# Kernel optimization log

Measured on AMD Instinct MI355X. Metric: run time of the kernel, lower is better.

Reference implementation:

```python
import jax, jax.numpy as jnp
import numpy as np


def _rope(x, fr, fi):
    # Faithful port of apply_rotary_embeddings: deinterleave even/odd elements,
    # reshape to (-1, *fr.shape), rotate, then concat halves and reshape back.
    shp = x.shape
    dims = fr.shape  # (seq_len, 1, head_dim//2)
    xf = x.reshape(-1, 2)
    xr = xf[:, 0].reshape((-1,) + dims)
    xi = xf[:, 1].reshape((-1,) + dims)
    out_r = xr * fr - xi * fi
    out_i = xr * fi + xi * fr
    return jnp.concatenate([out_r, out_i], axis=-1).reshape(shp).astype(x.dtype)


def setup_inputs() -> dict:
    key = jax.random.key(0)
    ks = jax.random.split(key, 9)
    B, S, Dm, H, Hd, P = 16, 1, 4096, 32, 128, 2048
    W = 0.02  # weight scale to keep score magnitudes sane
    return {
        "x": jax.random.normal(ks[0], (B, S, Dm), jnp.float32),
        "cache_k": jax.random.normal(ks[1], (B, P, H, Hd), jnp.float32),
        "cache_v": jax.random.normal(ks[2], (B, P, H, Hd), jnp.float32),
        "freqs_real": jax.random.normal(ks[3], (S, 1, Hd // 2), jnp.float32),
        "freqs_imag": jax.random.normal(ks[4], (S, 1, Hd // 2), jnp.float32),
        "dwq": jax.random.normal(ks[5], (Dm, Dm), jnp.float32) * W,
        "dwk": jax.random.normal(ks[6], (Dm, Dm), jnp.float32) * W,
        "dwv": jax.random.normal(ks[7], (Dm, Dm), jnp.float32) * W,
        "dwo": jax.random.normal(ks[8], (Dm, Dm), jnp.float32) * W,
        "start_pos": P,
    }


def reference(x, cache_k, cache_v, freqs_real, freqs_imag, dwq, dwk, dwv, dwo, start_pos):
    B, S, _ = x.shape
    H, Hd = cache_k.shape[2], cache_k.shape[3]
    scale = 1.0 / np.float32(np.sqrt(Hd))

    xq = (x @ dwq.T).reshape(B, S, H, Hd)
    xk = (x @ dwk.T).reshape(B, S, H, Hd)
    xv = (x @ dwv.T).reshape(B, S, H, Hd)
    xq = _rope(xq, freqs_real, freqs_imag)
    xk = _rope(xk, freqs_real, freqs_imag)

    # KV-cache append (cat-based growth in the original)
    keys = jnp.concatenate([cache_k, xk], axis=1)      # (B, P+S, H, Hd)
    values = jnp.concatenate([cache_v, xv], axis=1)

    q = xq.transpose(0, 2, 1, 3)       # (B, H, S, Hd)
    k = keys.transpose(0, 2, 1, 3)     # (B, H, P+S, Hd)
    v = values.transpose(0, 2, 1, 3)

    scores = jnp.einsum('bhqd,bhkd->bhqk', q, k) * scale
    probs = jax.nn.softmax(scores.astype(jnp.float32), axis=-1).astype(q.dtype)
    out = jnp.einsum('bhqk,bhkd->bhqd', probs, v)
    out = out.transpose(0, 2, 1, 3).reshape(B, S, H * Hd)
    return out @ dwo.T  # allreduce is identity with tp=1
```

## Files before the change

### kernel.cpp

```cpp
#include <hip/hip_runtime.h>
#include <cstdint>

#define DM 4096
#define NB 16
#define NH 32
#define HD 128
#define PP 2048
#define NCHUNK 32
#define CROWS 64
#define PSTRIDE 132
#define KP 256
#define NPAN (DM / KP)

typedef __attribute__((ext_vector_type(8))) short bf16x8;
typedef __attribute__((ext_vector_type(4))) float f32x4;

__device__ inline f32x4 ntld4(const float* p) {
  return __builtin_nontemporal_load(reinterpret_cast<const f32x4*>(p));
}

__device__ inline void split_pair(float x0, float x1, uint32_t& hpair,
                                  uint32_t& lpair) {
  uint32_t u0 = __float_as_uint(x0), u1 = __float_as_uint(x1);
  hpair = __builtin_amdgcn_perm(u1, u0, 0x07060302u);
  float l0 = x0 - __uint_as_float(u0 & 0xFFFF0000u);
  float l1 = x1 - __uint_as_float(u1 & 0xFFFF0000u);
  asm("v_cvt_pk_bf16_f32 %0, %1, %2" : "=v"(lpair) : "v"(l0), "v"(l1));
}

template <bool ROPE>
__device__ inline void gemv16(const float* __restrict__ A,
                              const float* __restrict__ W,
                              float* __restrict__ O, int jt,
                              const float* __restrict__ fr,
                              const float* __restrict__ fi) {
  const int wave = threadIdx.x >> 6;
  const int lane = threadIdx.x & 63;
  const int m = lane & 15;
  const int kg = lane >> 4;
  const float* arow = A + (size_t)m * DM;

  __shared__ float wt[2][16][KP + 4];
  __shared__ float red[4][256];

  f32x4 acc = {0.f, 0.f, 0.f, 0.f};

  {
    f32x4 s0[4];
#pragma unroll
    for (int j = 0; j < 4; ++j) {
      const int row = wave * 4 + j;
      s0[j] = ntld4(W + (size_t)(jt + row) * DM + lane * 4);
    }
#pragma unroll
    for (int j = 0; j < 4; ++j) {
      const int row = wave * 4 + j;
      *(f32x4*)&wt[0][row][lane * 4] = s0[j];
    }
  }
  __syncthreads();

  int buf = 0;
  for (int p = 0; p < NPAN; ++p) {
    f32x4 stg[4];
    if (p + 1 < NPAN) {
#pragma unroll
      for (int j = 0; j < 4; ++j) {
        const int row = wave * 4 + j;
        stg[j] = ntld4(W + (size_t)(jt + row) * DM + (p + 1) * KP + lane * 4);
      }
    }
#pragma unroll
    for (int s = 0; s < 2; ++s) {
      const int kl = (wave << 6) + (s << 5) + kg * 8;
      f32x4 wa = *(const f32x4*)&wt[buf][m][kl];
      f32x4 wb = *(const f32x4*)&wt[buf][m][kl + 4];
      f32x4 xa = *(const f32x4*)(arow + p * KP + kl);
      f32x4 xb = *(const f32x4*)(arow + p * KP + kl + 4);
      union { bf16x8 v; uint32_t d[4]; } ah, al, wh, wl;
      split_pair(xa.x, xa.y, ah.d[0], al.d[0]);
      split_pair(xa.z, xa.w, ah.d[1], al.d[1]);
      split_pair(xb.x, xb.y, ah.d[2], al.d[2]);
      split_pair(xb.z, xb.w, ah.d[3], al.d[3]);
      split_pair(wa.x, wa.y, wh.d[0], wl.d[0]);
      split_pair(wa.z, wa.w, wh.d[1], wl.d[1]);
      split_pair(wb.x, wb.y, wh.d[2], wl.d[2]);
      split_pair(wb.z, wb.w, wh.d[3], wl.d[3]);
      acc = __builtin_amdgcn_mfma_f32_16x16x32_bf16(ah.v, wh.v, acc, 0, 0, 0);
      acc = __builtin_amdgcn_mfma_f32_16x16x32_bf16(ah.v, wl.v, acc, 0, 0, 0);
      acc = __builtin_amdgcn_mfma_f32_16x16x32_bf16(al.v, wh.v, acc, 0, 0, 0);
    }
    if (p + 1 < NPAN) {
#pragma unroll
      for (int j = 0; j < 4; ++j) {
        const int row = wave * 4 + j;
        *(f32x4*)&wt[buf ^ 1][row][lane * 4] = stg[j];
      }
    }
    __syncthreads();
    buf ^= 1;
  }

  red[wave][lane * 4 + 0] = acc[0];
  red[wave][lane * 4 + 1] = acc[1];
  red[wave][lane * 4 + 2] = acc[2];
  red[wave][lane * 4 + 3] = acc[3];
  __syncthreads();
  const int t = threadIdx.x;
  float s = red[0][t] + red[1][t] + red[2][t] + red[3][t];
  float part = 0.f;
  if (ROPE) {
    __syncthreads();
    red[0][t] = s;
    __syncthreads();
    part = red[0][t ^ 4];
  }
  const int l = t >> 2, r = t & 3;
  const int bb = ((l >> 4) << 2) + r;
  const int n = l & 15;
  const int c = jt + n;
  float val;
  int oc;
  if (ROPE) {
    const int j = (c & 127) >> 1;
    const float f_r = fr[j], f_i = fi[j];
    if ((c & 1) == 0) {
      val = s * f_r - part * f_i;
      oc = (c & ~127) + j;
    } else {
      val = part * f_i + s * f_r;
      oc = (c & ~127) + 64 + j;
    }
  } else {
    val = s;
    oc = c;
  }
  O[(size_t)bb * DM + oc] = val;
}

__global__ __launch_bounds__(256) void qkv_proj_kernel(
    const float* __restrict__ x, const float* __restrict__ wq,
    const float* __restrict__ wk, const float* __restrict__ wv,
    const float* __restrict__ fr, const float* __restrict__ fi,
    float* __restrict__ oq, float* __restrict__ ok, float* __restrict__ ov) {
  const int g = blockIdx.x >> 8;
  const int jt = (blockIdx.x & 255) << 4;
  if (g == 0)
    gemv16<true>(x, wq, oq, jt, fr, fi);
  else if (g == 1)
    gemv16<true>(x, wk, ok, jt, fr, fi);
  else
    gemv16<false>(x, wv, ov, jt, nullptr, nullptr);
}

__global__ __launch_bounds__(256) void oproj_kernel(
    const float* __restrict__ a, const float* __restrict__ w,
    float* __restrict__ o) {
  gemv16<false>(a, w, o, blockIdx.x << 4, nullptr, nullptr);
}

__global__ __launch_bounds__(512) void attn_chunk_kernel(
    const float* __restrict__ qrope, const float* __restrict__ cache_k,
    const float* __restrict__ cache_v, float* __restrict__ part) {
  const int b = blockIdx.x >> 5;
  const int c = blockIdx.x & 31;
  const int t = threadIdx.x;
  __shared__ float sc[NH][CROWS];

  const f32x4 qa = *(const f32x4*)(qrope + (size_t)b * DM + 4 * t);
  const f32x4 qb = *(const f32x4*)(qrope + (size_t)b * DM + 2048 + 4 * t);
  const int h1 = t >> 5;
  const int h2 = h1 + 16;
  const float scale = 0.08838834764831845f;

  const float* Kb = cache_k + ((size_t)b * PP + (size_t)c * CROWS) * DM;
#pragma unroll 2
  for (int r = 0; r < CROWS; ++r) {
    const float* krow = Kb + (size_t)r * DM + 4 * t;
    f32x4 k1 = ntld4(krow);
    f32x4 k2 = ntld4(krow + 2048);
    float p1 = qa.x * k1.x + qa.y * k1.y + qa.z * k1.z + qa.w * k1.w;
    float p2 = qb.x * k2.x + qb.y * k2.y + qb.z * k2.z + qb.w * k2.w;
#pragma unroll
    for (int off = 1; off <= 16; off <<= 1) {
      p1 += __shfl_xor(p1, off);
      p2 += __shfl_xor(p2, off);
    }
    if ((t & 31) == 0) {
      sc[h1][r] = p1 * scale;
      sc[h2][r] = p2 * scale;
    }
  }
  __syncthreads();

  const int hh = t >> 4, u = t & 15;
  float4 sv4 = *(const float4*)(&sc[hh][u * 4]);
  float mx = fmaxf(fmaxf(sv4.x, sv4.y), fmaxf(sv4.z, sv4.w));
#pragma unroll
  for (int off = 1; off <= 8; off <<= 1) mx = fmaxf(mx, __shfl_xor(mx, off));
  float e0 = __expf(sv4.x - mx), e1 = __expf(sv4.y - mx);
  float e2 = __expf(sv4.z - mx), e3 = __expf(sv4.w - mx);
  float4 ev = {e0, e1, e2, e3};
  *(float4*)(&sc[hh][u * 4]) = ev;
  float sm = (e0 + e1) + (e2 + e3);
#pragma unroll
  for (int off = 1; off <= 8; off <<= 1) sm += __shfl_xor(sm, off);
  float* pb = part + ((size_t)(b * NCHUNK + c) * NH) * PSTRIDE;
  if (u == 0) {
    pb[hh * PSTRIDE + 128] = mx;
    pb[hh * PSTRIDE + 129] = sm;
  }
  __syncthreads();

  const float* Vb = cache_v + ((size_t)b * PP + (size_t)c * CROWS) * DM;
  f32x4 a1 = {0.f, 0.f, 0.f, 0.f}, a2 = {0.f, 0.f, 0.f, 0.f};
#pragma unroll 2
  for (int r = 0; r < CROWS; ++r) {
    const float* vrow = Vb + (size_t)r * DM + 4 * t;
    f32x4 v1 = ntld4(vrow);
    f32x4 v2 = ntld4(vrow + 2048);
    float w1 = sc[h1][r], w2 = sc[h2][r];
    a1 += w1 * v1;
    a2 += w2 * v2;
  }
  const int dbase = (4 * t) & 127;
  *(f32x4*)(pb + h1 * PSTRIDE + dbase) = a1;
  *(f32x4*)(pb + h2 * PSTRIDE + dbase) = a2;
}

__global__ __launch_bounds__(128) void attn_combine_kernel(
    const float* __restrict__ qrope, const float* __restrict__ krope,
    const float* __restrict__ vraw, const float* __restrict__ part,
    float* __restrict__ aout) {
  const int b = blockIdx.x >> 5;
  const int h = blockIdx.x & 31;
  const int d = threadIdx.x;
  __shared__ float red2[2];
  __shared__ float mv[NCHUNK], sv[NCHUNK], ec[NCHUNK];
  const size_t qoff = (size_t)b * DM + h * HD + d;
  float p = qrope[qoff] * krope[qoff];
#pragma unroll
  for (int off = 1; off <= 32; off <<= 1) p += __shfl_xor(p, off);
  if ((d & 63) == 0) red2[d >> 6] = p;
  const float* pb = part + ((size_t)b * NCHUNK * NH + h) * PSTRIDE;
  if (d < NCHUNK) {
    mv[d] = pb[(size_t)d * NH * PSTRIDE + 128];
    sv[d] = pb[(size_t)d * NH * PSTRIDE + 129];
  }
  __syncthreads();
  const float scale = 0.08838834764831845f;
  const float snew = (red2[0] + red2[1]) * scale;
  float M = snew;
#pragma unroll
  for (int c = 0; c < NCHUNK; ++c) M = fmaxf(M, mv[c]);
  if (d < NCHUNK) ec[d] = __expf(mv[d] - M);
  __syncthreads();
  const float en = __expf(snew - M);
  float S = en;
  float acc = en * vraw[qoff];
#pragma unroll 4
  for (int c = 0; c < NCHUNK; ++c) {
    acc += ec[c] * pb[(size_t)c * NH * PSTRIDE + d];
    S += ec[c] * sv[c];
  }
  aout[qoff] = acc / S;
}

extern "C" void kernel_launch(void* const* d_in, const int* in_sizes, int n_in,
                              void* d_out, int out_size, void* d_ws, size_t ws_size,
                              hipStream_t stream) {
  const float* x = (const float*)d_in[0];
  const float* cache_k = (const float*)d_in[1];
  const float* cache_v = (const float*)d_in[2];
  const float* fr = (const float*)d_in[3];
  const float* fi = (const float*)d_in[4];
  const float* dwq = (const float*)d_in[5];
  const float* dwk = (const float*)d_in[6];
  const float* dwv = (const float*)d_in[7];
  const float* dwo = (const float*)d_in[8];
  float* out = (float*)d_out;

  float* qrope = (float*)d_ws;
  float* krope = qrope + NB * DM;
  float* vraw = krope + NB * DM;
  float* aout = vraw + NB * DM;
  float* part = aout + NB * DM;

  qkv_proj_kernel<<<768, 256, 0, stream>>>(x, dwq, dwk, dwv, fr, fi,
                                           qrope, krope, vraw);
  attn_chunk_kernel<<<512, 512, 0, stream>>>(qrope, cache_k, cache_v, part);
  attn_combine_kernel<<<512, 128, 0, stream>>>(qrope, krope, vraw, part, aout);
  oproj_kernel<<<256, 256, 0, stream>>>(aout, dwo, out);
}
```

Before: 241.4 us.

## Fuse attention combine into chunk kernel with online softmax and deeper GEMV prefetch

The attention chunk kernel now streams K and V rows in a single loop and keeps online-softmax running max and sum, which removes the shared-memory score buffer and the separate V pass. The last block for each batch, found with an atomic counter that the QKV kernel resets, performs the cross-chunk combine, so the separate combine kernel launch goes away. The GEMV loop is unrolled by two panels with two register staging sets, so the weight prefetch runs two panels ahead. The trade-offs are more exp calls per row, more registers, and the cost of the atomic and fence.

```diff
diff --git a/kernel.cpp b/kernel.cpp
--- a/kernel.cpp
+++ b/kernel.cpp
@@ -42,64 +42,73 @@
 
   __shared__ float wt[2][16][KP + 4];
   __shared__ float red[4][256];
-
   f32x4 acc = {0.f, 0.f, 0.f, 0.f};
+
+#define GROW(j) (W + (size_t)(jt + wave * 4 + (j)) * DM)
+#define COMPUTE(P, BI)                                                        \
+  {                                                                           \
+    _Pragma("unroll") for (int s = 0; s < 2; ++s) {                           \
+      const int kl = (wave << 6) + (s << 5) + kg * 8;                         \
+      f32x4 wa = *(const f32x4*)&wt[BI][m][kl];                               \
+      f32x4 wb = *(const f32x4*)&wt[BI][m][kl + 4];                           \
+      f32x4 xa = *(const f32x4*)(arow + (P)*KP + kl);                         \
+      f32x4 xb = *(const f32x4*)(arow + (P)*KP + kl + 4);                     \
+      union { bf16x8 v; uint32_t d[4]; } ah, al, wh, wl;                      \
+      split_pair(xa.x, xa.y, ah.d[0], al.d[0]);                               \
+      split_pair(xa.z, xa.w, ah.d[1], al.d[1]);                               \
+      split_pair(xb.x, xb.y, ah.d[2], al.d[2]);                               \
+      split_pair(xb.z, xb.w, ah.d[3], al.d[3]);                               \
+      split_pair(wa.x, wa.y, wh.d[0], wl.d[0]);                               \
+      split_pair(wa.z, wa.w, wh.d[1], wl.d[1]);                               \
+      split_pair(wb.x, wb.y, wh.d[2], wl.d[2]);                               \
+      split_pair(wb.z, wb.w, wh.d[3], wl.d[3]);                               \
+      acc = __builtin_amdgcn_mfma_f32_16x16x32_bf16(ah.v, wh.v, acc, 0, 0, 0);\
+      acc = __builtin_amdgcn_mfma_f32_16x16x32_bf16(ah.v, wl.v, acc, 0, 0, 0);\
+      acc = __builtin_amdgcn_mfma_f32_16x16x32_bf16(al.v, wh.v, acc, 0, 0, 0);\
+    }                                                                         \
+  }
 
   {
     f32x4 s0[4];
 #pragma unroll
-    for (int j = 0; j < 4; ++j) {
-      const int row = wave * 4 + j;
-      s0[j] = ntld4(W + (size_t)(jt + row) * DM + lane * 4);
-    }
-#pragma unroll
-    for (int j = 0; j < 4; ++j) {
-      const int row = wave * 4 + j;
-      *(f32x4*)&wt[0][row][lane * 4] = s0[j];
-    }
-  }
+    for (int j = 0; j < 4; ++j) s0[j] = ntld4(GROW(j) + lane * 4);
+#pragma unroll
+    for (int j = 0; j < 4; ++j)
+      *(f32x4*)&wt[0][wave * 4 + j][lane * 4] = s0[j];
+  }
+  f32x4 sA[4], sB[4];
+#pragma unroll
+  for (int j = 0; j < 4; ++j) sA[j] = ntld4(GROW(j) + KP + lane * 4);
   __syncthreads();
 
-  int buf = 0;
-  for (int p = 0; p < NPAN; ++p) {
-    f32x4 stg[4];
-    if (p + 1 < NPAN) {
-#pragma unroll
-      for (int j = 0; j < 4; ++j) {
-        const int row = wave * 4 + j;
-        stg[j] = ntld4(W + (size_t)(jt + row) * DM + (p + 1) * KP + lane * 4);
-      }
-    }
-#pragma unroll
-    for (int s = 0; s < 2; ++s) {
-      const int kl = (wave << 6) + (s << 5) + kg * 8;
-      f32x4 wa = *(const f32x4*)&wt[buf][m][kl];
-      f32x4 wb = *(const f32x4*)&wt[buf][m][kl + 4];
-      f32x4 xa = *(const f32x4*)(arow + p * KP + kl);
-      f32x4 xb = *(const f32x4*)(arow + p * KP + kl + 4);
-      union { bf16x8 v; uint32_t d[4]; } ah, al, wh, wl;
-      split_pair(xa.x, xa.y, ah.d[0], al.d[0]);
-      split_pair(xa.z, xa.w, ah.d[1], al.d[1]);
-      split_pair(xb.x, xb.y, ah.d[2], al.d[2]);
-      split_pair(xb.z, xb.w, ah.d[3], al.d[3]);
-      split_pair(wa.x, wa.y, wh.d[0], wl.d[0]);
-      split_pair(wa.z, wa.w, wh.d[1], wl.d[1]);
-      split_pair(wb.x, wb.y, wh.d[2], wl.d[2]);
-      split_pair(wb.z, wb.w, wh.d[3], wl.d[3]);
-      acc = __builtin_amdgcn_mfma_f32_16x16x32_bf16(ah.v, wh.v, acc, 0, 0, 0);
-      acc = __builtin_amdgcn_mfma_f32_16x16x32_bf16(ah.v, wl.v, acc, 0, 0, 0);
-      acc = __builtin_amdgcn_mfma_f32_16x16x32_bf16(al.v, wh.v, acc, 0, 0, 0);
-    }
-    if (p + 1 < NPAN) {
-#pragma unroll
-      for (int j = 0; j < 4; ++j) {
-        const int row = wave * 4 + j;
-        *(f32x4*)&wt[buf ^ 1][row][lane * 4] = stg[j];
-      }
-    }
+  for (int k = 0; k < NPAN / 2; ++k) {
+    const int p0 = 2 * k;
+    if (p0 + 2 < NPAN) {
+#pragma unroll
+      for (int j = 0; j < 4; ++j)
+        sB[j] = ntld4(GROW(j) + (p0 + 2) * KP + lane * 4);
+    }
+    COMPUTE(p0, 0);
+#pragma unroll
+    for (int j = 0; j < 4; ++j)
+      *(f32x4*)&wt[1][wave * 4 + j][lane * 4] = sA[j];
     __syncthreads();
-    buf ^= 1;
-  }
+    const int p1 = p0 + 1;
+    if (p1 + 2 < NPAN) {
+#pragma unroll
+      for (int j = 0; j < 4; ++j)
+        sA[j] = ntld4(GROW(j) + (p1 + 2) * KP + lane * 4);
+    }
+    COMPUTE(p1, 1);
+    if (p1 + 1 < NPAN) {
+#pragma unroll
+      for (int j = 0; j < 4; ++j)
+        *(f32x4*)&wt[0][wave * 4 + j][lane * 4] = sB[j];
+    }
+    __syncthreads();
+  }
+#undef GROW
+#undef COMPUTE
 
   red[wave][lane * 4 + 0] = acc[0];
   red[wave][lane * 4 + 1] = acc[1];
@@ -142,7 +151,9 @@
     const float* __restrict__ x, const float* __restrict__ wq,
     const float* __restrict__ wk, const float* __restrict__ wv,
     const float* __restrict__ fr, const float* __restrict__ fi,
-    float* __restrict__ oq, float* __restrict__ ok, float* __restrict__ ov) {
+    float* __restrict__ oq, float* __restrict__ ok, float* __restrict__ ov,
+    int* __restrict__ cnt) {
+  if (blockIdx.x == 0 && threadIdx.x < NB) cnt[threadIdx.x] = 0;
   const int g = blockIdx.x >> 8;
   const int jt = (blockIdx.x & 255) << 4;
   if (g == 0)
@@ -160,25 +171,31 @@
 }
 
 __global__ __launch_bounds__(512) void attn_chunk_kernel(
-    const float* __restrict__ qrope, const float* __restrict__ cache_k,
-    const float* __restrict__ cache_v, float* __restrict__ part) {
+    const float* __restrict__ qrope, const float* __restrict__ krope,
+    const float* __restrict__ vraw, const float* __restrict__ cache_k,
+    const float* __restrict__ cache_v, float* __restrict__ part,
+    int* __restrict__ cnt, float* __restrict__ aout) {
   const int b = blockIdx.x >> 5;
   const int c = blockIdx.x & 31;
   const int t = threadIdx.x;
-  __shared__ float sc[NH][CROWS];
-
   const f32x4 qa = *(const f32x4*)(qrope + (size_t)b * DM + 4 * t);
   const f32x4 qb = *(const f32x4*)(qrope + (size_t)b * DM + 2048 + 4 * t);
-  const int h1 = t >> 5;
-  const int h2 = h1 + 16;
+  const int h1 = t >> 5, h2 = h1 + 16;
   const float scale = 0.08838834764831845f;
 
   const float* Kb = cache_k + ((size_t)b * PP + (size_t)c * CROWS) * DM;
+  const float* Vb = cache_v + ((size_t)b * PP + (size_t)c * CROWS) * DM;
+
+  float m1 = -1e30f, s1 = 0.f, m2 = -1e30f, s2 = 0.f;
+  f32x4 a1 = {0.f, 0.f, 0.f, 0.f}, a2 = {0.f, 0.f, 0.f, 0.f};
 #pragma unroll 2
   for (int r = 0; r < CROWS; ++r) {
     const float* krow = Kb + (size_t)r * DM + 4 * t;
+    const float* vrow = Vb + (size_t)r * DM + 4 * t;
     f32x4 k1 = ntld4(krow);
     f32x4 k2 = ntld4(krow + 2048);
+    f32x4 v1 = ntld4(vrow);
+    f32x4 v2 = ntld4(vrow + 2048);
     float p1 = qa.x * k1.x + qa.y * k1.y + qa.z * k1.z + qa.w * k1.w;
     float p2 = qb.x * k2.x + qb.y * k2.y + qb.z * k2.z + qb.w * k2.w;
 #pragma unroll
@@ -186,84 +203,74 @@
       p1 += __shfl_xor(p1, off);
       p2 += __shfl_xor(p2, off);
     }
-    if ((t & 31) == 0) {
-      sc[h1][r] = p1 * scale;
-      sc[h2][r] = p2 * scale;
-    }
-  }
-  __syncthreads();
-
-  const int hh = t >> 4, u = t & 15;
-  float4 sv4 = *(const float4*)(&sc[hh][u * 4]);
-  float mx = fmaxf(fmaxf(sv4.x, sv4.y), fmaxf(sv4.z, sv4.w));
-#pragma unroll
-  for (int off = 1; off <= 8; off <<= 1) mx = fmaxf(mx, __shfl_xor(mx, off));
-  float e0 = __expf(sv4.x - mx), e1 = __expf(sv4.y - mx);
-  float e2 = __expf(sv4.z - mx), e3 = __expf(sv4.w - mx);
-  float4 ev = {e0, e1, e2, e3};
-  *(float4*)(&sc[hh][u * 4]) = ev;
-  float sm = (e0 + e1) + (e2 + e3);
-#pragma unroll
-  for (int off = 1; off <= 8; off <<= 1) sm += __shfl_xor(sm, off);
-  float* pb = part + ((size_t)(b * NCHUNK + c) * NH) * PSTRIDE;
-  if (u == 0) {
-    pb[hh * PSTRIDE + 128] = mx;
-    pb[hh * PSTRIDE + 129] = sm;
-  }
-  __syncthreads();
-
-  const float* Vb = cache_v + ((size_t)b * PP + (size_t)c * CROWS) * DM;
-  f32x4 a1 = {0.f, 0.f, 0.f, 0.f}, a2 = {0.f, 0.f, 0.f, 0.f};
-#pragma unroll 2
-  for (int r = 0; r < CROWS; ++r) {
-    const float* vrow = Vb + (size_t)r * DM + 4 * t;
-    f32x4 v1 = ntld4(vrow);
-    f32x4 v2 = ntld4(vrow + 2048);
-    float w1 = sc[h1][r], w2 = sc[h2][r];
-    a1 += w1 * v1;
-    a2 += w2 * v2;
-  }
+    p1 *= scale;
+    p2 *= scale;
+    float n1 = fmaxf(m1, p1);
+    float c1 = __expf(m1 - n1), w1 = __expf(p1 - n1);
+    s1 = s1 * c1 + w1;
+    a1 = a1 * c1 + w1 * v1;
+    m1 = n1;
+    float n2 = fmaxf(m2, p2);
+    float c2 = __expf(m2 - n2), w2 = __expf(p2 - n2);
+    s2 = s2 * c2 + w2;
+    a2 = a2 * c2 + w2 * v2;
+    m2 = n2;
+  }
+  float* pb = part + (size_t)(b * NCHUNK + c) * NH * PSTRIDE;
   const int dbase = (4 * t) & 127;
   *(f32x4*)(pb + h1 * PSTRIDE + dbase) = a1;
   *(f32x4*)(pb + h2 * PSTRIDE + dbase) = a2;
-}
-
-__global__ __launch_bounds__(128) void attn_combine_kernel(
-    const float* __restrict__ qrope, const float* __restrict__ krope,
-    const float* __restrict__ vraw, const float* __restrict__ part,
-    float* __restrict__ aout) {
-  const int b = blockIdx.x >> 5;
-  const int h = blockIdx.x & 31;
-  const int d = threadIdx.x;
-  __shared__ float red2[2];
-  __shared__ float mv[NCHUNK], sv[NCHUNK], ec[NCHUNK];
-  const size_t qoff = (size_t)b * DM + h * HD + d;
-  float p = qrope[qoff] * krope[qoff];
-#pragma unroll
-  for (int off = 1; off <= 32; off <<= 1) p += __shfl_xor(p, off);
-  if ((d & 63) == 0) red2[d >> 6] = p;
-  const float* pb = part + ((size_t)b * NCHUNK * NH + h) * PSTRIDE;
-  if (d < NCHUNK) {
-    mv[d] = pb[(size_t)d * NH * PSTRIDE + 128];
-    sv[d] = pb[(size_t)d * NH * PSTRIDE + 129];
-  }
+  if ((t & 31) == 0) {
+    pb[h1 * PSTRIDE + 128] = m1;
+    pb[h1 * PSTRIDE + 129] = s1;
+    pb[h2 * PSTRIDE + 128] = m2;
+    pb[h2 * PSTRIDE + 129] = s2;
+  }
+
   __syncthreads();
-  const float scale = 0.08838834764831845f;
-  const float snew = (red2[0] + red2[1]) * scale;
+  __shared__ int lastf;
+  if (t == 0) {
+    __threadfence();
+    lastf = (atomicAdd(&cnt[b], 1) == NCHUNK - 1) ? 1 : 0;
+  }
+  __syncthreads();
+  if (!lastf) return;
+  __threadfence();
+
+  const int h = t >> 4;
+  const int d0 = (t & 15) * 8;
+  const size_t qo = (size_t)b * DM + h * HD + d0;
+  float pd = 0.f;
+#pragma unroll
+  for (int j = 0; j < 8; ++j) pd += qrope[qo + j] * krope[qo + j];
+  pd += __shfl_xor(pd, 1);
+  pd += __shfl_xor(pd, 2);
+  pd += __shfl_xor(pd, 4);
+  pd += __shfl_xor(pd, 8);
+  const float snew = pd * scale;
+  const float* pball = part + (size_t)b * NCHUNK * NH * PSTRIDE + h * PSTRIDE;
   float M = snew;
-#pragma unroll
-  for (int c = 0; c < NCHUNK; ++c) M = fmaxf(M, mv[c]);
-  if (d < NCHUNK) ec[d] = __expf(mv[d] - M);
-  __syncthreads();
+#pragma unroll 4
+  for (int cc = 0; cc < NCHUNK; ++cc)
+    M = fmaxf(M, pball[(size_t)cc * NH * PSTRIDE + 128]);
   const float en = __expf(snew - M);
   float S = en;
-  float acc = en * vraw[qoff];
+  f32x4 A1 = {0.f, 0.f, 0.f, 0.f}, A2 = {0.f, 0.f, 0.f, 0.f};
 #pragma unroll 4
-  for (int c = 0; c < NCHUNK; ++c) {
-    acc += ec[c] * pb[(size_t)c * NH * PSTRIDE + d];
-    S += ec[c] * sv[c];
-  }
-  aout[qoff] = acc / S;
+  for (int cc = 0; cc < NCHUNK; ++cc) {
+    const float* pc = pball + (size_t)cc * NH * PSTRIDE;
+    float e = __expf(pc[128] - M);
+    S += e * pc[129];
+    A1 += e * *(const f32x4*)(pc + d0);
+    A2 += e * *(const f32x4*)(pc + d0 + 4);
+  }
+  f32x4 vn1 = *(const f32x4*)(vraw + qo);
+  f32x4 vn2 = *(const f32x4*)(vraw + qo + 4);
+  A1 += en * vn1;
+  A2 += en * vn2;
+  const float inv = 1.0f / S;
+  *(f32x4*)(aout + qo) = A1 * inv;
+  *(f32x4*)(aout + qo + 4) = A2 * inv;
 }
 
 extern "C" void kernel_launch(void* const* d_in, const int* in_sizes, int n_in,
@@ -285,10 +292,11 @@
   float* vraw = krope + NB * DM;
   float* aout = vraw + NB * DM;
   float* part = aout + NB * DM;
+  int* cnt = (int*)(part + (size_t)NB * NCHUNK * NH * PSTRIDE);
 
   qkv_proj_kernel<<<768, 256, 0, stream>>>(x, dwq, dwk, dwv, fr, fi,
-                                           qrope, krope, vraw);
-  attn_chunk_kernel<<<512, 512, 0, stream>>>(qrope, cache_k, cache_v, part);
-  attn_combine_kernel<<<512, 128, 0, stream>>>(qrope, krope, vraw, part, aout);
+                                           qrope, krope, vraw, cnt);
+  attn_chunk_kernel<<<512, 512, 0, stream>>>(qrope, krope, vraw, cache_k,
+                                             cache_v, part, cnt, aout);
   oproj_kernel<<<256, 256, 0, stream>>>(aout, dwo, out);
 }
```

After: 315.8 us. +30.8%, slower.
